# Optimization experiments

Measured on AMD Instinct MI355X. Metric: run time of the kernel, lower is better.

Reference implementation:

```python
import jax, jax.numpy as jnp
import numpy as np

VOCAB, EMBED, HIDDEN, NCLS = 32000, 512, 1024, 1000
BATCH, SEQ = 128, 512


def setup_inputs() -> dict:
    key = jax.random.key(0)
    ks = jax.random.split(key, 8)
    s_in = 1.0 / np.sqrt(EMBED + HIDDEN)
    s_h = 1.0 / np.sqrt(HIDDEN)
    return {
        "x": jax.random.randint(ks[0], (BATCH, SEQ), 0, VOCAB, dtype=jnp.int32),
        "emb": jax.random.normal(ks[1], (VOCAB, EMBED), dtype=jnp.float32),
        "Wz": jax.random.uniform(ks[2], (EMBED + HIDDEN, HIDDEN), jnp.float32, -s_in, s_in),
        "bz": jax.random.uniform(ks[3], (HIDDEN,), jnp.float32, -s_in, s_in),
        "Wh": jax.random.uniform(ks[4], (EMBED + HIDDEN, HIDDEN), jnp.float32, -s_in, s_in),
        "bh": jax.random.uniform(ks[5], (HIDDEN,), jnp.float32, -s_in, s_in),
        "Wfc": jax.random.uniform(ks[6], (HIDDEN, NCLS), jnp.float32, -s_h, s_h),
        "bfc": jax.random.uniform(ks[7], (NCLS,), jnp.float32, -s_h, s_h),
    }


def reference(x, emb, Wz, bz, Wh, bh, Wfc, bfc):
    # embedding lookup: [B, S, E]
    e = emb[x]
    B = x.shape[0]
    h0 = jnp.zeros((B, Wz.shape[1]), dtype=emb.dtype)

    def step(h, x_t):
        c = jnp.concatenate([x_t, h], axis=1)          # [B, E+H]
        z = jax.nn.sigmoid(c @ Wz + bz)                # forget/update gate
        h_tilde = jnp.tanh(c @ Wh + bh)                # candidate state
        h_new = (1.0 - z) * h + z * h_tilde
        return h_new, None

    h_final, _ = jax.lax.scan(step, h0, jnp.swapaxes(e, 0, 1))  # scan over S
    return h_final @ Wfc + bfc                          # logits [B, NCLS]
```

## Files before the change

kernel.cpp:

```cpp
#include <hip/hip_runtime.h>

#define BATCH 128
#define SEQ   512
#define EMB   512
#define HID   1024
#define NCLS  1000
#define NBLK  128
#define TPB   512

using short8 = __attribute__((ext_vector_type(8))) short;
using f32x4  = __attribute__((ext_vector_type(4))) float;
typedef unsigned long long u64;

__device__ __forceinline__ short f2bf(float f) {
    unsigned u = __float_as_uint(f);
    unsigned r = (u + 0x7fffu + ((u >> 16) & 1u)) >> 16;
    return (short)r;
}
__device__ __forceinline__ float bf2f(short s) {
    unsigned u = ((unsigned)(unsigned short)s) << 16;
    return __uint_as_float(u);
}
__device__ __forceinline__ short8 pack8(float4 a, float4 b) {
    short8 s;
    s[0] = f2bf(a.x); s[1] = f2bf(a.y); s[2] = f2bf(a.z); s[3] = f2bf(a.w);
    s[4] = f2bf(b.x); s[5] = f2bf(b.y); s[6] = f2bf(b.z); s[7] = f2bf(b.w);
    return s;
}
__device__ __forceinline__ short8 mk8(u64 lo, u64 hi) {
    union { u64 d[2]; short8 s; } u;
    u.d[0] = lo; u.d[1] = hi;
    return u.s;
}

#define OFF_CH0 0u
#define OFF_CL0 262144u
#define OFF_BAR 524288u
#define OFF_CH1 526336u
#define OFF_CL1 788480u
#define OFF_H   1050624u
#define ZERO_I4 32896u

__global__ void mgu_init(int4* __restrict__ ws4) {
    unsigned i = blockIdx.x * blockDim.x + threadIdx.x;
    if (i < ZERO_I4) ws4[i] = make_int4(0, 0, 0, 0);
}

__global__ __launch_bounds__(TPB, 1) void mgu_scan(
    const int* __restrict__ x, const float* __restrict__ emb,
    const float* __restrict__ Wz, const float* __restrict__ bz,
    const float* __restrict__ Wh, const float* __restrict__ bh,
    short* __restrict__ ch0, short* __restrict__ cl0,
    short* __restrict__ ch1, short* __restrict__ cl1,
    unsigned* __restrict__ bars, float* __restrict__ h)
{
    __shared__ f32x4 Rbuf[8][8][64];

    const int tid  = threadIdx.x;
    const int w    = tid >> 6;
    const int lane = tid & 63;
    const int q    = lane >> 4;
    const int n    = lane & 15;
    const int blk  = blockIdx.x;
    const int r0   = (blk >> 4) << 4;
    const int jb   = (blk & 15) << 6;
    const int j0   = jb + (w << 3);
    unsigned* bar  = bars + ((blk >> 4) << 6);

    const float* Wg = (n < 8) ? Wz : Wh;
    short8 Bf[48];
#pragma unroll
    for (int c = 0; c < 8; ++c) {
#pragma unroll
        for (int m = 0; m < 6; ++m) {
            const float* wp = Wg + jb + (c << 3) + (n & 7);
            short8 f;
#pragma unroll
            for (int i = 0; i < 8; ++i)
                f[i] = f2bf(wp[(long)((w + 8 * m) * 32 + q * 8 + i) * HID]);
            Bf[c * 6 + m] = f;
        }
    }
    const float bzv = bz[j0 + (n & 7)];
    const float bhv = bh[j0 + (n & 7)];

    float hreg[4] = {0.f, 0.f, 0.f, 0.f};

    const int xrow = (r0 + n) * SEQ;
    const int hoff = (r0 + n) * HID + (w << 5) + (q << 3);
    const int eoff = (w << 5) + (q << 3);

    short8 fe0, fe1;
    {
        int tok = x[xrow];
        const float* ep = emb + (long)tok * EMB + eoff;
        float4 a0 = *(const float4*)(ep);
        float4 a1 = *(const float4*)(ep + 4);
        float4 b0 = *(const float4*)(ep + 256);
        float4 b1 = *(const float4*)(ep + 260);
        fe0 = pack8(a0, a1);
        fe1 = pack8(b0, b1);
    }

    for (int t = 0; t < SEQ; ++t) {
        const short* chR = (t & 1) ? ch1 : ch0;
        const short* clR = (t & 1) ? cl1 : cl0;
        short*       chW = (t & 1) ? ch0 : ch1;
        short*       clW = (t & 1) ? cl0 : cl1;

        int tok_nxt = x[xrow + ((t < SEQ - 1) ? t + 1 : t)];

        u64 hh[8], ll[8];
#pragma unroll
        for (int mm = 0; mm < 4; ++mm) {
            const u64* hp = (const u64*)(chR + hoff + (mm << 8));
            hh[2 * mm]     = __hip_atomic_load(hp,     __ATOMIC_RELAXED, __HIP_MEMORY_SCOPE_AGENT);
            hh[2 * mm + 1] = __hip_atomic_load(hp + 1, __ATOMIC_RELAXED, __HIP_MEMORY_SCOPE_AGENT);
        }
#pragma unroll
        for (int mm = 0; mm < 4; ++mm) {
            const u64* lp = (const u64*)(clR + hoff + (mm << 8));
            ll[2 * mm]     = __hip_atomic_load(lp,     __ATOMIC_RELAXED, __HIP_MEMORY_SCOPE_AGENT);
            ll[2 * mm + 1] = __hip_atomic_load(lp + 1, __ATOMIC_RELAXED, __HIP_MEMORY_SCOPE_AGENT);
        }

        f32x4 acc[8];
#pragma unroll
        for (int c = 0; c < 8; ++c) acc[c] = (f32x4){0.f, 0.f, 0.f, 0.f};

#pragma unroll
        for (int c = 0; c < 8; ++c)
            acc[c] = __builtin_amdgcn_mfma_f32_16x16x32_bf16(fe0, Bf[c * 6 + 0], acc[c], 0, 0, 0);
#pragma unroll
        for (int c = 0; c < 8; ++c)
            acc[c] = __builtin_amdgcn_mfma_f32_16x16x32_bf16(fe1, Bf[c * 6 + 1], acc[c], 0, 0, 0);

#pragma unroll
        for (int mm = 0; mm < 4; ++mm) {
            short8 fh = mk8(hh[2 * mm], hh[2 * mm + 1]);
#pragma unroll
            for (int c = 0; c < 8; ++c)
                acc[c] = __builtin_amdgcn_mfma_f32_16x16x32_bf16(fh, Bf[c * 6 + 2 + mm], acc[c], 0, 0, 0);
        }
#pragma unroll
        for (int mm = 0; mm < 4; ++mm) {
            short8 fl = mk8(ll[2 * mm], ll[2 * mm + 1]);
#pragma unroll
            for (int c = 0; c < 8; ++c)
                acc[c] = __builtin_amdgcn_mfma_f32_16x16x32_bf16(fl, Bf[c * 6 + 2 + mm], acc[c], 0, 0, 0);
        }

#pragma unroll
        for (int c = 0; c < 8; ++c) Rbuf[w][c][lane] = acc[c];
        __syncthreads();
        f32x4 r = Rbuf[0][w][lane];
#pragma unroll
        for (int w2 = 1; w2 < 8; ++w2) r += Rbuf[w2][w][lane];

        float oarr[4];
        oarr[0] = __shfl_xor(r[0], 8, 64);
        oarr[1] = __shfl_xor(r[1], 8, 64);
        oarr[2] = __shfl_xor(r[2], 8, 64);
        oarr[3] = __shfl_xor(r[3], 8, 64);

        if (n < 8) {
            const int j = j0 + n;
#pragma unroll
            for (int r2 = 0; r2 < 4; ++r2) {
                float z  = 1.f / (1.f + __expf(-(r[r2] + bzv)));
                float ht = tanhf(oarr[r2] + bhv);
                float ho = hreg[r2];
                float hn = ho + z * (ht - ho);
                hreg[r2] = hn;
                int rr = (r0 + q * 4 + r2) * HID + j;
                if (t < SEQ - 1) {
                    short hi = f2bf(hn);
                    __hip_atomic_store(chW + rr, hi, __ATOMIC_RELAXED, __HIP_MEMORY_SCOPE_AGENT);
                    __hip_atomic_store(clW + rr, f2bf(hn - bf2f(hi)), __ATOMIC_RELAXED, __HIP_MEMORY_SCOPE_AGENT);
                } else {
                    h[rr] = hn;
                }
            }
        }

        if (t < SEQ - 1) {
            __syncthreads();
            if (tid == 0)
                __hip_atomic_fetch_add(bar, 1u, __ATOMIC_RELAXED, __HIP_MEMORY_SCOPE_AGENT);
            {
                const float* ep = emb + (long)tok_nxt * EMB + eoff;
                float4 a0 = *(const float4*)(ep);
                float4 a1 = *(const float4*)(ep + 4);
                float4 b0 = *(const float4*)(ep + 256);
                float4 b1 = *(const float4*)(ep + 260);
                fe0 = pack8(a0, a1);
                fe1 = pack8(b0, b1);
            }
            if (tid == 0) {
                unsigned tgt = (unsigned)(t + 1) * 16u;
                while (__hip_atomic_load(bar, __ATOMIC_RELAXED, __HIP_MEMORY_SCOPE_AGENT) < tgt)
                    __builtin_amdgcn_s_sleep(1);
            }
            __syncthreads();
        }
    }
}

__global__ __launch_bounds__(256) void mgu_fc(const float* __restrict__ h,
                                              const float* __restrict__ Wfc,
                                              const float* __restrict__ bfc,
                                              float* __restrict__ out) {
    __shared__ float hs[BATCH][65];
    const int tid = threadIdx.x;
    const int n0  = blockIdx.x * 8;
    const int b   = tid & 127;
    const int nn  = tid >> 7;
    const int nc  = n0 + nn * 4;
    float acc0 = 0.f, acc1 = 0.f, acc2 = 0.f, acc3 = 0.f;

    for (int k0 = 0; k0 < HID; k0 += 64) {
        __syncthreads();
#pragma unroll
        for (int jj = 0; jj < 8; ++jj) {
            int idx = tid + jj * 256;
            int bb  = idx >> 4;
            int kk  = (idx & 15) << 2;
            const float4 v = *(const float4*)(h + bb * HID + k0 + kk);
            hs[bb][kk] = v.x; hs[bb][kk + 1] = v.y; hs[bb][kk + 2] = v.z; hs[bb][kk + 3] = v.w;
        }
        __syncthreads();
#pragma unroll 8
        for (int k = 0; k < 64; ++k) {
            float hv = hs[b][k];
            const float4 wv = *(const float4*)(Wfc + (long)(k0 + k) * NCLS + nc);
            acc0 += hv * wv.x; acc1 += hv * wv.y; acc2 += hv * wv.z; acc3 += hv * wv.w;
        }
    }
    float* op = out + b * NCLS + nc;
    op[0] = acc0 + bfc[nc + 0];
    op[1] = acc1 + bfc[nc + 1];
    op[2] = acc2 + bfc[nc + 2];
    op[3] = acc3 + bfc[nc + 3];
}

extern "C" void kernel_launch(void* const* d_in, const int* in_sizes, int n_in,
                              void* d_out, int out_size, void* d_ws, size_t ws_size,
                              hipStream_t stream) {
    const int*   x   = (const int*)  d_in[0];
    const float* emb = (const float*)d_in[1];
    const float* Wz  = (const float*)d_in[2];
    const float* bz  = (const float*)d_in[3];
    const float* Wh  = (const float*)d_in[4];
    const float* bh  = (const float*)d_in[5];
    const float* Wfc = (const float*)d_in[6];
    const float* bfc = (const float*)d_in[7];
    float* out = (float*)d_out;

    char* ws = (char*)d_ws;
    short*    ch0  = (short*)   (ws + OFF_CH0);
    short*    cl0  = (short*)   (ws + OFF_CL0);
    unsigned* bars = (unsigned*)(ws + OFF_BAR);
    short*    ch1  = (short*)   (ws + OFF_CH1);
    short*    cl1  = (short*)   (ws + OFF_CL1);
    float*    h    = (float*)   (ws + OFF_H);

    mgu_init<<<129, 256, 0, stream>>>((int4*)ws);

    mgu_scan<<<NBLK, TPB, 0, stream>>>(x, emb, Wz, bz, Wh, bh,
                                       ch0, cl0, ch1, cl1, bars, h);

    mgu_fc<<<125, 256, 0, stream>>>(h, Wfc, bfc, out);
}
```

Measured before the change: 4.276 ms.

## Replace counter barrier with per-element tagged hidden-state exchange

Removes the per-group atomic counter barrier and the polling loop. Each hidden-state element is now written as a 64-bit word that carries the step number as a tag next to the packed bf16 hi/lo pair. Consumers poll their own fragment loads until every tag matches, and they overlap the embedding MFMAs with that wait. A double-buffered LDS reduction buffer drops one __syncthreads per step, and producers write in an MFMA-fragment layout gathered through LDS. In exchange the exchange traffic doubles and spinning happens on full vector loads.

```diff
diff --git a/kernel.cpp b/kernel.cpp
--- a/kernel.cpp
+++ b/kernel.cpp
@@ -27,19 +27,11 @@
     s[4] = f2bf(b.x); s[5] = f2bf(b.y); s[6] = f2bf(b.z); s[7] = f2bf(b.w);
     return s;
 }
-__device__ __forceinline__ short8 mk8(u64 lo, u64 hi) {
-    union { u64 d[2]; short8 s; } u;
-    u.d[0] = lo; u.d[1] = hi;
-    return u.s;
-}
-
-#define OFF_CH0 0u
-#define OFF_CL0 262144u
-#define OFF_BAR 524288u
-#define OFF_CH1 526336u
-#define OFF_CL1 788480u
-#define OFF_H   1050624u
-#define ZERO_I4 32896u
+
+#define OFF_EX0 0u
+#define OFF_EX1 1048576u
+#define OFF_H   2097152u
+#define ZERO_I4 131072u
 
 __global__ void mgu_init(int4* __restrict__ ws4) {
     unsigned i = blockIdx.x * blockDim.x + threadIdx.x;
@@ -50,11 +42,10 @@
     const int* __restrict__ x, const float* __restrict__ emb,
     const float* __restrict__ Wz, const float* __restrict__ bz,
     const float* __restrict__ Wh, const float* __restrict__ bh,
-    short* __restrict__ ch0, short* __restrict__ cl0,
-    short* __restrict__ ch1, short* __restrict__ cl1,
-    unsigned* __restrict__ bars, float* __restrict__ h)
+    u64* __restrict__ ex0, u64* __restrict__ ex1, float* __restrict__ h)
 {
-    __shared__ f32x4 Rbuf[8][8][64];
+    __shared__ f32x4    Rbuf[2][8][8][64];
+    __shared__ unsigned TrP[8][16][8];
 
     const int tid  = threadIdx.x;
     const int w    = tid >> 6;
@@ -65,7 +56,9 @@
     const int r0   = (blk >> 4) << 4;
     const int jb   = (blk & 15) << 6;
     const int j0   = jb + (w << 3);
-    unsigned* bar  = bars + ((blk >> 4) << 6);
+    const int frg  = (blk >> 4) * 16384;
+    const int ksw  = ((blk & 15) << 1) + (w >> 2);
+    const int qw   = w & 3;
 
     const float* Wg = (n < 8) ? Wz : Wh;
     short8 Bf[48];
@@ -87,7 +80,6 @@
     float hreg[4] = {0.f, 0.f, 0.f, 0.f};
 
     const int xrow = (r0 + n) * SEQ;
-    const int hoff = (r0 + n) * HID + (w << 5) + (q << 3);
     const int eoff = (w << 5) + (q << 3);
 
     short8 fe0, fe1;
@@ -103,26 +95,24 @@
     }
 
     for (int t = 0; t < SEQ; ++t) {
-        const short* chR = (t & 1) ? ch1 : ch0;
-        const short* clR = (t & 1) ? cl1 : cl0;
-        short*       chW = (t & 1) ? ch0 : ch1;
-        short*       clW = (t & 1) ? cl0 : cl1;
+        const u64* EXr = (t & 1) ? ex1 : ex0;
+        u64*       EXw = (t & 1) ? ex0 : ex1;
+        const unsigned want = (unsigned)t;
 
         int tok_nxt = x[xrow + ((t < SEQ - 1) ? t + 1 : t)];
 
-        u64 hh[8], ll[8];
-#pragma unroll
-        for (int mm = 0; mm < 4; ++mm) {
-            const u64* hp = (const u64*)(chR + hoff + (mm << 8));
-            hh[2 * mm]     = __hip_atomic_load(hp,     __ATOMIC_RELAXED, __HIP_MEMORY_SCOPE_AGENT);
-            hh[2 * mm + 1] = __hip_atomic_load(hp + 1, __ATOMIC_RELAXED, __HIP_MEMORY_SCOPE_AGENT);
-        }
-#pragma unroll
-        for (int mm = 0; mm < 4; ++mm) {
-            const u64* lp = (const u64*)(clR + hoff + (mm << 8));
-            ll[2 * mm]     = __hip_atomic_load(lp,     __ATOMIC_RELAXED, __HIP_MEMORY_SCOPE_AGENT);
-            ll[2 * mm + 1] = __hip_atomic_load(lp + 1, __ATOMIC_RELAXED, __HIP_MEMORY_SCOPE_AGENT);
-        }
+        u64 ev[32];
+        const u64* fp0 = EXr + frg + (lane << 2);
+#define LOADF                                                                         \
+        _Pragma("unroll")                                                             \
+        for (int mm = 0; mm < 4; ++mm) {                                              \
+            const u64* fp = fp0 + (w + 8 * mm) * 512;                                 \
+            _Pragma("unroll")                                                         \
+            for (int i = 0; i < 8; ++i)                                               \
+                ev[mm * 8 + i] = __hip_atomic_load(fp + (i >> 2) * 256 + (i & 3),     \
+                                   __ATOMIC_RELAXED, __HIP_MEMORY_SCOPE_AGENT);       \
+        }
+        LOADF
 
         f32x4 acc[8];
 #pragma unroll
@@ -135,27 +125,39 @@
         for (int c = 0; c < 8; ++c)
             acc[c] = __builtin_amdgcn_mfma_f32_16x16x32_bf16(fe1, Bf[c * 6 + 1], acc[c], 0, 0, 0);
 
+        for (;;) {
+            bool ok = true;
+#pragma unroll
+            for (int k2 = 0; k2 < 32; ++k2)
+                ok = ok && ((unsigned)(ev[k2] >> 32) == want);
+            if (__all(ok)) break;
+            LOADF
+        }
+#undef LOADF
+
 #pragma unroll
         for (int mm = 0; mm < 4; ++mm) {
-            short8 fh = mk8(hh[2 * mm], hh[2 * mm + 1]);
+            short8 fh, fl;
+#pragma unroll
+            for (int i = 0; i < 8; ++i) {
+                unsigned lo32 = (unsigned)ev[mm * 8 + i];
+                fh[i] = (short)(unsigned short)(lo32 >> 16);
+                fl[i] = (short)(unsigned short)(lo32 & 0xffffu);
+            }
 #pragma unroll
             for (int c = 0; c < 8; ++c)
                 acc[c] = __builtin_amdgcn_mfma_f32_16x16x32_bf16(fh, Bf[c * 6 + 2 + mm], acc[c], 0, 0, 0);
-        }
-#pragma unroll
-        for (int mm = 0; mm < 4; ++mm) {
-            short8 fl = mk8(ll[2 * mm], ll[2 * mm + 1]);
 #pragma unroll
             for (int c = 0; c < 8; ++c)
                 acc[c] = __builtin_amdgcn_mfma_f32_16x16x32_bf16(fl, Bf[c * 6 + 2 + mm], acc[c], 0, 0, 0);
         }
 
 #pragma unroll
-        for (int c = 0; c < 8; ++c) Rbuf[w][c][lane] = acc[c];
+        for (int c = 0; c < 8; ++c) Rbuf[t & 1][w][c][lane] = acc[c];
         __syncthreads();
-        f32x4 r = Rbuf[0][w][lane];
-#pragma unroll
-        for (int w2 = 1; w2 < 8; ++w2) r += Rbuf[w2][w][lane];
+        f32x4 r = Rbuf[t & 1][0][w][lane];
+#pragma unroll
+        for (int w2 = 1; w2 < 8; ++w2) r += Rbuf[t & 1][w2][w][lane];
 
         float oarr[4];
         oarr[0] = __shfl_xor(r[0], 8, 64);
@@ -172,36 +174,31 @@
                 float ho = hreg[r2];
                 float hn = ho + z * (ht - ho);
                 hreg[r2] = hn;
-                int rr = (r0 + q * 4 + r2) * HID + j;
                 if (t < SEQ - 1) {
                     short hi = f2bf(hn);
-                    __hip_atomic_store(chW + rr, hi, __ATOMIC_RELAXED, __HIP_MEMORY_SCOPE_AGENT);
-                    __hip_atomic_store(clW + rr, f2bf(hn - bf2f(hi)), __ATOMIC_RELAXED, __HIP_MEMORY_SCOPE_AGENT);
+                    short lo = f2bf(hn - bf2f(hi));
+                    TrP[w][q * 4 + r2][n] =
+                        ((unsigned)(unsigned short)hi << 16) | (unsigned short)lo;
                 } else {
-                    h[rr] = hn;
+                    h[(r0 + q * 4 + r2) * HID + j] = hn;
                 }
             }
         }
 
         if (t < SEQ - 1) {
-            __syncthreads();
-            if (tid == 0)
-                __hip_atomic_fetch_add(bar, 1u, __ATOMIC_RELAXED, __HIP_MEMORY_SCOPE_AGENT);
-            {
-                const float* ep = emb + (long)tok_nxt * EMB + eoff;
-                float4 a0 = *(const float4*)(ep);
-                float4 a1 = *(const float4*)(ep + 4);
-                float4 b0 = *(const float4*)(ep + 256);
-                float4 b1 = *(const float4*)(ep + 260);
-                fe0 = pack8(a0, a1);
-                fe1 = pack8(b0, b1);
-            }
-            if (tid == 0) {
-                unsigned tgt = (unsigned)(t + 1) * 16u;
-                while (__hip_atomic_load(bar, __ATOMIC_RELAXED, __HIP_MEMORY_SCOPE_AGENT) < tgt)
-                    __builtin_amdgcn_s_sleep(1);
-            }
-            __syncthreads();
+            const u64 tagw = ((u64)(unsigned)(t + 1)) << 32;
+            u64* sp = EXw + frg + ksw * 512 + qw * 64 + lane;
+            unsigned h0 = TrP[w][lane >> 2][(lane & 3)];
+            unsigned h1 = TrP[w][lane >> 2][4 + (lane & 3)];
+            __hip_atomic_store(sp,       tagw | h0, __ATOMIC_RELAXED, __HIP_MEMORY_SCOPE_AGENT);
+            __hip_atomic_store(sp + 256, tagw | h1, __ATOMIC_RELAXED, __HIP_MEMORY_SCOPE_AGENT);
+            const float* ep = emb + (long)tok_nxt * EMB + eoff;
+            float4 a0 = *(const float4*)(ep);
+            float4 a1 = *(const float4*)(ep + 4);
+            float4 b0 = *(const float4*)(ep + 256);
+            float4 b1 = *(const float4*)(ep + 260);
+            fe0 = pack8(a0, a1);
+            fe1 = pack8(b0, b1);
         }
     }
 }
@@ -257,17 +254,13 @@
     float* out = (float*)d_out;
 
     char* ws = (char*)d_ws;
-    short*    ch0  = (short*)   (ws + OFF_CH0);
-    short*    cl0  = (short*)   (ws + OFF_CL0);
-    unsigned* bars = (unsigned*)(ws + OFF_BAR);
-    short*    ch1  = (short*)   (ws + OFF_CH1);
-    short*    cl1  = (short*)   (ws + OFF_CL1);
-    float*    h    = (float*)   (ws + OFF_H);
-
-    mgu_init<<<129, 256, 0, stream>>>((int4*)ws);
-
-    mgu_scan<<<NBLK, TPB, 0, stream>>>(x, emb, Wz, bz, Wh, bh,
-                                       ch0, cl0, ch1, cl1, bars, h);
+    u64*   ex0 = (u64*)  (ws + OFF_EX0);
+    u64*   ex1 = (u64*)  (ws + OFF_EX1);
+    float* h   = (float*)(ws + OFF_H);
+
+    mgu_init<<<512, 256, 0, stream>>>((int4*)ws);
+
+    mgu_scan<<<NBLK, TPB, 0, stream>>>(x, emb, Wz, bz, Wh, bh, ex0, ex1, h);
 
     mgu_fc<<<125, 256, 0, stream>>>(h, Wfc, bfc, out);
 }
```

Result: slower. 9.411 ms (+120.1%).
